# Optimization experiments

Measured on AMD Instinct MI355X. Metric: run time of the kernel, lower is better.

Reference implementation:

```python
import jax, jax.numpy as jnp
import numpy as np

B, S, U, V, L = 64, 2048, 1024, 50257, 8
RESIDUAL = (False, False, True, True, True, True, True, False)


def setup_inputs() -> dict:
    key = jax.random.key(0)
    ks = jax.random.split(key, 8)
    sc = 0.02
    return {
        "enc_output": jax.random.normal(ks[0], (B, S, U), jnp.float32),
        "dec_input": jax.random.normal(ks[1], (B, 1, U), jnp.float32),
        "query_h": jax.random.normal(ks[2], (B, U), jnp.float32),
        "attn_W1": jax.random.normal(ks[3], (U, U), jnp.float32) * sc,
        "attn_b1": jnp.zeros((U,), jnp.float32),
        "attn_W2": jax.random.normal(ks[4], (U, U), jnp.float32) * sc,
        "attn_b2": jnp.zeros((U,), jnp.float32),
        "attn_V": jax.random.normal(ks[5], (U, 1), jnp.float32) * sc,
        "attn_bV": jnp.zeros((1,), jnp.float32),
        "lstm_W": jax.random.normal(ks[6], (L, 2 * U, 4 * U), jnp.float32) * sc,
        "lstm_b": jnp.zeros((L, 4 * U), jnp.float32),
        "dense_W": jax.random.normal(ks[7], (U, V), jnp.float32) * sc,
        "dense_b": jnp.zeros((V,), jnp.float32),
    }


def reference(enc_output, dec_input, query_h, attn_W1, attn_b1, attn_W2, attn_b2,
              attn_V, attn_bV, lstm_W, lstm_b, dense_W, dense_b):
    # Bahdanau attention: score over the S (time) axis of enc_output
    feat = jnp.tanh(jnp.einsum('bsu,uv->bsv', enc_output, attn_W1) + attn_b1
                    + (query_h @ attn_W2 + attn_b2)[:, None, :])          # [B,S,U]
    score = jnp.einsum('bsu,uo->bso', feat, attn_V) + attn_bV             # [B,S,1]
    attn_w = jax.nn.softmax(score, axis=1)                                # [B,S,1]
    ctx = jnp.sum(attn_w * enc_output, axis=1)                            # [B,U]

    # 8 stacked single-step LSTMs. NOTE: original code never passes
    # initial_state, so h_prev = c_prev = 0 and the recurrent kernel
    # contributes exactly zero for a length-1 sequence.
    x = dec_input[:, 0, :]                                                # [B,U]
    hs, cs = [], []
    for i in range(L):
        inp = jnp.concatenate([x, ctx], axis=-1)                          # [B,2U]
        z = inp @ lstm_W[i] + lstm_b[i]                                   # [B,4U]
        i_g, f_g, g_g, o_g = jnp.split(z, 4, axis=-1)                     # keras order i,f,c,o
        c = jax.nn.sigmoid(i_g) * jnp.tanh(g_g)                           # f*c_prev == 0
        h = jax.nn.sigmoid(o_g) * jnp.tanh(c)
        hs.append(h)
        cs.append(c)
        x = h + inp[:, :U] if RESIDUAL[i] else h                          # residual on layers 2..6

    logits = x @ dense_W + dense_b                                        # [B,V]
    probs = jax.nn.softmax(logits, axis=-1)[:, None, :]                   # [B,1,V]
    return probs, jnp.stack(hs), jnp.stack(cs), attn_w
```

## Files before the change

kernel.cpp:

```cpp
#include <hip/hip_runtime.h>
#include <stdint.h>

#define B_  64
#define S_  2048
#define U_  1024
#define V_  50257
#define L_  8

typedef __attribute__((ext_vector_type(4))) float  f32x4;
typedef __attribute__((ext_vector_type(8))) short  bf16x8;
typedef __attribute__((ext_vector_type(4))) unsigned short us4;

__device__ inline unsigned short f2bf(float f){
  union { float f; unsigned u; } x; x.f = f;
  unsigned r = (x.u + 0x7FFFu + ((x.u >> 16) & 1u)) >> 16;
  return (unsigned short)r;
}
__device__ inline float fast_tanh(float x){
  float e = __expf(2.0f * x);
  return (e - 1.0f) * __builtin_amdgcn_rcpf(e + 1.0f);
}
__device__ inline void gload_lds16(const void* g, void* l){
  __builtin_amdgcn_global_load_lds(
      (const __attribute__((address_space(1))) unsigned int*)g,
      (__attribute__((address_space(3))) unsigned int*)l, 16, 0, 0);
}

__global__ void k1a_w1t(const float* __restrict__ W1, unsigned short* __restrict__ W1T){
  __shared__ float tile[64][65];
  int bu = blockIdx.x & 15, bv = blockIdx.x >> 4;
  int u0 = bu * 64, v0 = bv * 64;
  int t = threadIdx.x;
  int r = t >> 6, c = t & 63;
  #pragma unroll 4
  for (int it = 0; it < 16; ++it){
    int rr = it * 4 + r;
    tile[rr][c] = W1[(long)(u0 + rr) * 1024 + v0 + c];
  }
  __syncthreads();
  #pragma unroll 4
  for (int it = 0; it < 16; ++it){
    int vr = it * 4 + r;
    W1T[(long)(v0 + vr) * 1024 + u0 + c] = f2bf(tile[c][vr]);
  }
}

__global__ void k1b_qbias(const float* __restrict__ qh, const float* __restrict__ W2,
                          const float* __restrict__ b1, const float* __restrict__ b2,
                          float* __restrict__ qbias){
  int b = blockIdx.x >> 2;
  int v = (blockIdx.x & 3) * 256 + threadIdx.x;
  const float* qr = qh + b * 1024;
  float a = 0.f;
  for (int j = 0; j < 256; ++j){
    f32x4 qv = *(const f32x4*)(qr + j * 4);
    a += qv[0] * W2[(long)(j*4+0)*1024 + v] + qv[1] * W2[(long)(j*4+1)*1024 + v]
       + qv[2] * W2[(long)(j*4+2)*1024 + v] + qv[3] * W2[(long)(j*4+3)*1024 + v];
  }
  qbias[b * 1024 + v] = a + b1[v] + b2[v];
}

#define K2T 512
__global__ __launch_bounds__(K2T, 2) void k2_feat_score(
    const float* __restrict__ enc, const unsigned short* __restrict__ W1T,
    const float* __restrict__ qbias, const float* __restrict__ attnV,
    float* __restrict__ score){
  __shared__ __attribute__((aligned(16))) unsigned short Bs[1024 * 64];
  __shared__ __attribute__((aligned(16))) unsigned short As[64 * 136];
  __shared__ float qbL[1024], vwL[1024], scoreL[64];

  const int tid  = threadIdx.x;
  const int lane = tid & 63;
  const int w    = tid >> 6;
  const int blk  = blockIdx.x;
  const long row0 = (long)blk * 64;
  const int b = blk >> 5;

  for (int i = tid; i < 1024; i += K2T){ qbL[i] = qbias[b*1024 + i]; vwL[i] = attnV[i]; }
  if (tid < 64) scoreL[tid] = 0.0f;

  f32x4 acc[4][8];
  #pragma unroll
  for (int mi = 0; mi < 4; ++mi)
    #pragma unroll
    for (int ni = 0; ni < 8; ++ni) acc[mi][ni] = (f32x4){0.f,0.f,0.f,0.f};

  int goff[16];
  #pragma unroll
  for (int it = 0; it < 16; ++it){
    int d = it * 512 + tid;
    int v = d >> 3, c = d & 7;
    goff[it] = v * 1024 + (c ^ (v & 7)) * 8;
  }

  for (int p = 0; p < 8; ++p){
    __syncthreads();
    {
      const float* src = enc + row0 * 1024 + p * 128;
      #pragma unroll
      for (int it = 0; it < 4; ++it){
        int idx = it * 512 + tid;
        int r = idx >> 5, c4 = idx & 31;
        f32x4 v4 = *(const f32x4*)(src + (long)r * 1024 + c4 * 4);
        us4 sv;
        sv[0] = f2bf(v4[0]); sv[1] = f2bf(v4[1]); sv[2] = f2bf(v4[2]); sv[3] = f2bf(v4[3]);
        *(us4*)&As[r * 136 + c4 * 4] = sv;
      }
    }
    #pragma unroll
    for (int s2 = 0; s2 < 2; ++s2){
      __syncthreads();
      const int kk = p * 128 + s2 * 64;
      #pragma unroll
      for (int it = 0; it < 16; ++it){
        int dbase = it * 512 + w * 64;
        gload_lds16(W1T + goff[it] + kk, &Bs[dbase * 8]);
      }
      __syncthreads();
      #pragma unroll
      for (int k0 = 0; k0 < 2; ++k0){
        bf16x8 af[4];
        #pragma unroll
        for (int mi = 0; mi < 4; ++mi){
          int r = mi * 16 + (lane & 15);
          int kloc = s2 * 64 + k0 * 32 + (lane >> 4) * 8;
          af[mi] = *(const bf16x8*)&As[r * 136 + kloc];
        }
        #pragma unroll
        for (int ni = 0; ni < 8; ++ni){
          int v = w * 128 + ni * 16 + (lane & 15);
          int c = k0 * 4 + (lane >> 4);
          bf16x8 bf = *(const bf16x8*)&Bs[v * 64 + (c ^ (v & 7)) * 8];
          #pragma unroll
          for (int mi = 0; mi < 4; ++mi)
            acc[mi][ni] = __builtin_amdgcn_mfma_f32_16x16x32_bf16(af[mi], bf, acc[mi][ni], 0, 0, 0);
        }
      }
    }
  }
  float qv[8], vv[8];
  #pragma unroll
  for (int ni = 0; ni < 8; ++ni){
    int col = w * 128 + ni * 16 + (lane & 15);
    qv[ni] = qbL[col]; vv[ni] = vwL[col];
  }
  #pragma unroll
  for (int mi = 0; mi < 4; ++mi){
    #pragma unroll
    for (int r = 0; r < 4; ++r){
      float t = 0.f;
      #pragma unroll
      for (int ni = 0; ni < 8; ++ni)
        t += fast_tanh(acc[mi][ni][r] + qv[ni]) * vv[ni];
      #pragma unroll
      for (int off = 1; off < 16; off <<= 1) t += __shfl_xor(t, off, 16);
      if ((lane & 15) == 0)
        atomicAdd(&scoreL[mi * 16 + (lane >> 4) * 4 + r], t);
    }
  }
  __syncthreads();
  if (tid < 64) score[row0 + tid] = scoreL[tid];
}

__global__ void k3_softmax_s(const float* __restrict__ score, float* __restrict__ attnw){
  __shared__ float red[256];
  int b = blockIdx.x, t = threadIdx.x;
  const float* sc = score + b * 2048;
  float m = -1e30f;
  for (int i = t; i < 2048; i += 256) m = fmaxf(m, sc[i]);
  red[t] = m; __syncthreads();
  for (int s = 128; s > 0; s >>= 1){ if (t < s) red[t] = fmaxf(red[t], red[t+s]); __syncthreads(); }
  float M = red[0]; __syncthreads();
  float p = 0.f;
  for (int i = t; i < 2048; i += 256) p += __expf(sc[i] - M);
  red[t] = p; __syncthreads();
  for (int s = 128; s > 0; s >>= 1){ if (t < s) red[t] += red[t+s]; __syncthreads(); }
  float inv = 1.0f / red[0];
  for (int i = t; i < 2048; i += 256) attnw[b * 2048 + i] = __expf(sc[i] - M) * inv;
}

__global__ void k4_ctx(const float* __restrict__ enc, const float* __restrict__ attnw,
                       float* __restrict__ ctx){
  __shared__ float wL[2048];
  __shared__ f32x4 red[8][32];
  int b = blockIdx.x >> 3, uc = blockIdx.x & 7;
  int t = threadIdx.x;
  for (int i = t; i < 2048; i += 256) wL[i] = attnw[b * 2048 + i];
  __syncthreads();
  int g = t >> 5, l32 = t & 31;
  const float* base = enc + (long)b * 2048 * 1024 + uc * 128 + l32 * 4;
  f32x4 a = (f32x4){0.f,0.f,0.f,0.f};
  for (int s = g; s < 2048; s += 8){
    f32x4 e = *(const f32x4*)(base + (long)s * 1024);
    a += e * wL[s];
  }
  red[g][l32] = a; __syncthreads();
  if (g == 0){
    f32x4 r = red[0][l32];
    #pragma unroll
    for (int i = 1; i < 8; ++i) r += red[i][l32];
    *(f32x4*)(ctx + b * 1024 + uc * 128 + l32 * 4) = r;
  }
}

__global__ void k5a_gemm(const float* __restrict__ x, const float* __restrict__ ctx,
                         const float* __restrict__ W, float* __restrict__ zpart){
  __shared__ float inpL[64 * 256];
  int blk = blockIdx.x;
  int nc = blk % 48, ks = blk / 48;
  int t = threadIdx.x;
  int gc = (nc < 16) ? nc * 64 : (nc < 32 ? 2048 + (nc - 16) * 64 : 3072 + (nc - 32) * 64);
  const float* ib = (ks < 4) ? x : ctx;
  int koff = (ks & 3) * 256;
  #pragma unroll 4
  for (int it = 0; it < 16; ++it){
    int idx = it * 256 + t;
    int r = idx >> 6, c4 = idx & 63;
    *(f32x4*)&inpL[r * 256 + c4 * 4] = *(const f32x4*)(ib + (long)r * 1024 + koff + c4 * 4);
  }
  __syncthreads();
  int b4 = (t & 15) * 4, n4 = (t >> 4) * 4;
  f32x4 a0 = (f32x4){0,0,0,0}, a1 = a0, a2 = a0, a3 = a0;
  const float* Wb = W + (long)(ks * 256) * 4096 + gc + n4;
  #pragma unroll 2
  for (int j = 0; j < 64; ++j){
    f32x4 w0 = *(const f32x4*)(Wb + (long)(j*4+0) * 4096);
    f32x4 w1 = *(const f32x4*)(Wb + (long)(j*4+1) * 4096);
    f32x4 w2 = *(const f32x4*)(Wb + (long)(j*4+2) * 4096);
    f32x4 w3 = *(const f32x4*)(Wb + (long)(j*4+3) * 4096);
    f32x4 x0 = *(const f32x4*)&inpL[(b4+0) * 256 + j * 4];
    f32x4 x1 = *(const f32x4*)&inpL[(b4+1) * 256 + j * 4];
    f32x4 x2 = *(const f32x4*)&inpL[(b4+2) * 256 + j * 4];
    f32x4 x3 = *(const f32x4*)&inpL[(b4+3) * 256 + j * 4];
    a0 += w0*x0[0]; a0 += w1*x0[1]; a0 += w2*x0[2]; a0 += w3*x0[3];
    a1 += w0*x1[0]; a1 += w1*x1[1]; a1 += w2*x1[2]; a1 += w3*x1[3];
    a2 += w0*x2[0]; a2 += w1*x2[1]; a2 += w2*x2[2]; a2 += w3*x2[3];
    a3 += w0*x3[0]; a3 += w1*x3[1]; a3 += w2*x3[2]; a3 += w3*x3[3];
  }
  float* zp = zpart + (long)ks * 64 * 3072 + nc * 64 + n4;
  *(f32x4*)(zp + (long)(b4+0) * 3072) = a0;
  *(f32x4*)(zp + (long)(b4+1) * 3072) = a1;
  *(f32x4*)(zp + (long)(b4+2) * 3072) = a2;
  *(f32x4*)(zp + (long)(b4+3) * 3072) = a3;
}

__global__ void k5b_gates(const float* __restrict__ zpart, const float* __restrict__ lb,
                          const float* __restrict__ xin, float* __restrict__ xout,
                          float* __restrict__ hs, float* __restrict__ cs, int resid){
  int b = blockIdx.x, t = threadIdx.x;
  int n4 = t * 4;
  f32x4 zi = (f32x4){0,0,0,0}, zg = zi, zo = zi;
  #pragma unroll
  for (int ks = 0; ks < 8; ++ks){
    const float* zp = zpart + (long)ks * 64 * 3072 + b * 3072;
    zi += *(const f32x4*)(zp + n4);
    zg += *(const f32x4*)(zp + 1024 + n4);
    zo += *(const f32x4*)(zp + 2048 + n4);
  }
  zi += *(const f32x4*)(lb + n4);
  zg += *(const f32x4*)(lb + 2048 + n4);
  zo += *(const f32x4*)(lb + 3072 + n4);
  f32x4 c, h;
  #pragma unroll
  for (int j = 0; j < 4; ++j){
    float cv = (1.f / (1.f + __expf(-zi[j]))) * tanhf(zg[j]);
    float hv = (1.f / (1.f + __expf(-zo[j]))) * tanhf(cv);
    c[j] = cv; h[j] = hv;
  }
  f32x4 xn = h;
  if (resid) xn += *(const f32x4*)(xin + b * 1024 + n4);
  *(f32x4*)(hs + b * 1024 + n4) = h;
  *(f32x4*)(cs + b * 1024 + n4) = c;
  *(f32x4*)(xout + b * 1024 + n4) = xn;
}

__global__ void k6_dense(const float* __restrict__ x, const float* __restrict__ dW,
                         const float* __restrict__ db, float* __restrict__ logits){
  int nc = blockIdx.x, t = threadIdx.x;
  int b4 = (t & 15) * 4, nl = (t >> 4) * 4;
  int col = nc * 64 + nl;
  int c0 = min(col + 0, V_ - 1), c1 = min(col + 1, V_ - 1);
  int c2 = min(col + 2, V_ - 1), c3 = min(col + 3, V_ - 1);
  f32x4 a[4];
  #pragma unroll
  for (int bi = 0; bi < 4; ++bi) a[bi] = (f32x4){0,0,0,0};
  for (int j = 0; j < 256; ++j){
    f32x4 xv0 = *(const f32x4*)(x + (long)(b4+0) * 1024 + j * 4);
    f32x4 xv1 = *(const f32x4*)(x + (long)(b4+1) * 1024 + j * 4);
    f32x4 xv2 = *(const f32x4*)(x + (long)(b4+2) * 1024 + j * 4);
    f32x4 xv3 = *(const f32x4*)(x + (long)(b4+3) * 1024 + j * 4);
    #pragma unroll
    for (int ki = 0; ki < 4; ++ki){
      const float* wr = dW + (long)(j * 4 + ki) * V_;
      f32x4 wv = { wr[c0], wr[c1], wr[c2], wr[c3] };
      a[0] += wv * xv0[ki]; a[1] += wv * xv1[ki];
      a[2] += wv * xv2[ki]; a[3] += wv * xv3[ki];
    }
  }
  f32x4 bias = { db[c0], db[c1], db[c2], db[c3] };
  #pragma unroll
  for (int bi = 0; bi < 4; ++bi){
    f32x4 r = a[bi] + bias;
    #pragma unroll
    for (int j = 0; j < 4; ++j)
      if (col + j < V_) logits[(long)(b4 + bi) * V_ + col + j] = r[j];
  }
}

__global__ void k7_softmax_v(const float* __restrict__ logits, float* __restrict__ probs){
  __shared__ float red[1024];
  int b = blockIdx.x, t = threadIdx.x;
  const float* lg = logits + (long)b * V_;
  float* pr = probs + (long)b * V_;
  float m = -1e30f;
  for (int i = t; i < V_; i += 1024) m = fmaxf(m, lg[i]);
  red[t] = m; __syncthreads();
  for (int s = 512; s > 0; s >>= 1){ if (t < s) red[t] = fmaxf(red[t], red[t+s]); __syncthreads(); }
  float M = red[0]; __syncthreads();
  float p = 0.f;
  for (int i = t; i < V_; i += 1024){ float e = __expf(lg[i] - M); pr[i] = e; p += e; }
  red[t] = p; __syncthreads();
  for (int s = 512; s > 0; s >>= 1){ if (t < s) red[t] += red[t+s]; __syncthreads(); }
  float inv = 1.0f / red[0];
  for (int i = t; i < V_; i += 1024) pr[i] *= inv;
}

extern "C" void kernel_launch(void* const* d_in, const int* in_sizes, int n_in,
                              void* d_out, int out_size, void* d_ws, size_t ws_size,
                              hipStream_t stream){
  const float* enc = (const float*)d_in[0];
  const float* dec = (const float*)d_in[1];
  const float* qh  = (const float*)d_in[2];
  const float* W1  = (const float*)d_in[3];
  const float* b1  = (const float*)d_in[4];
  const float* W2  = (const float*)d_in[5];
  const float* b2  = (const float*)d_in[6];
  const float* aV  = (const float*)d_in[7];
  const float* lW  = (const float*)d_in[9];
  const float* lb  = (const float*)d_in[10];
  const float* dW  = (const float*)d_in[11];
  const float* db  = (const float*)d_in[12];

  float* out   = (float*)d_out;
  float* probs = out;
  float* hs    = out + 3216448;
  float* cs    = out + 3740736;
  float* attnw = out + 4265024;

  char* ws = (char*)d_ws;
  unsigned short* W1T = (unsigned short*)(ws + 0);
  float* score  = (float*)(ws + 2097152);
  float* qbias  = (float*)(ws + 2621440);
  float* ctx    = (float*)(ws + 2883584);
  float* xbuf   = (float*)(ws + 3145728);
  float* zpart  = (float*)(ws + 3407872);
  float* logits = (float*)(ws + 9699328);

  hipLaunchKernelGGL(k1a_w1t,      dim3(256),  dim3(256),  0, stream, W1, W1T);
  hipLaunchKernelGGL(k1b_qbias,    dim3(256),  dim3(256),  0, stream, qh, W2, b1, b2, qbias);
  hipLaunchKernelGGL(k2_feat_score,dim3(2048), dim3(K2T),  0, stream, enc, W1T, qbias, aV, score);
  hipLaunchKernelGGL(k3_softmax_s, dim3(64),   dim3(256),  0, stream, score, attnw);
  hipLaunchKernelGGL(k4_ctx,       dim3(512),  dim3(256),  0, stream, enc, attnw, ctx);

  static const int RES[8] = {0,0,1,1,1,1,1,0};
  const float* xin = dec;
  for (int i = 0; i < 8; ++i){
    hipLaunchKernelGGL(k5a_gemm,  dim3(384), dim3(256), 0, stream,
                       xin, ctx, lW + (long)i * 2048 * 4096, zpart);
    hipLaunchKernelGGL(k5b_gates, dim3(64),  dim3(256), 0, stream,
                       zpart, lb + i * 4096, xin, xbuf,
                       hs + i * 65536, cs + i * 65536, RES[i]);
    xin = xbuf;
  }
  hipLaunchKernelGGL(k6_dense,     dim3(786), dim3(256),  0, stream, xbuf, dW, db, logits);
  hipLaunchKernelGGL(k7_softmax_v, dim3(64),  dim3(1024), 0, stream, logits, probs);
}
```

Baseline: 2.898 ms.

## Double-buffer attention GEMM, repack W1 tiles, split ctx reduction, retile dense

The attention feature GEMM now double-buffers A and B tiles in LDS with K-step 32. The next tile's W1 load (direct-to-LDS) and the enc row load are issued while the MFMAs on the current tile run, and there is one barrier per step. W1 is pre-packed into contiguous swizzled 32-wide K tiles so each step reads a linear block. The context reduction is split over S chunks with a second reduce kernel, and the dense layer is retiled so each thread computes 16 batch rows for one column with coalesced weight reads. zpart and logits now share workspace, which relies on the two never being live at the same time.

Result: faster. 2.516 ms (-13.2%).

```diff
diff --git a/kernel.cpp b/kernel.cpp
--- a/kernel.cpp
+++ b/kernel.cpp
@@ -10,6 +10,7 @@
 typedef __attribute__((ext_vector_type(4))) float  f32x4;
 typedef __attribute__((ext_vector_type(8))) short  bf16x8;
 typedef __attribute__((ext_vector_type(4))) unsigned short us4;
+typedef __attribute__((ext_vector_type(8))) unsigned short us8;
 
 __device__ inline unsigned short f2bf(float f){
   union { float f; unsigned u; } x; x.f = f;
@@ -26,22 +27,28 @@
       (__attribute__((address_space(3))) unsigned int*)l, 16, 0, 0);
 }
 
-__global__ void k1a_w1t(const float* __restrict__ W1, unsigned short* __restrict__ W1T){
-  __shared__ float tile[64][65];
-  int bu = blockIdx.x & 15, bv = blockIdx.x >> 4;
-  int u0 = bu * 64, v0 = bv * 64;
+__global__ void k1a_w1b(const float* __restrict__ W1, unsigned short* __restrict__ W1B){
+  __shared__ float tile[32][257];
+  int tt = blockIdx.x >> 2;
+  int v0 = (blockIdx.x & 3) * 256;
   int t = threadIdx.x;
-  int r = t >> 6, c = t & 63;
   #pragma unroll 4
-  for (int it = 0; it < 16; ++it){
-    int rr = it * 4 + r;
-    tile[rr][c] = W1[(long)(u0 + rr) * 1024 + v0 + c];
-  }
-  __syncthreads();
-  #pragma unroll 4
-  for (int it = 0; it < 16; ++it){
-    int vr = it * 4 + r;
-    W1T[(long)(v0 + vr) * 1024 + u0 + c] = f2bf(tile[c][vr]);
+  for (int i = 0; i < 32; ++i){
+    int idx = i * 256 + t;
+    int r = idx >> 8, c = idx & 255;
+    tile[r][c] = W1[(long)(tt * 32 + r) * 1024 + v0 + c];
+  }
+  __syncthreads();
+  #pragma unroll
+  for (int i = 0; i < 4; ++i){
+    int gid = i * 256 + t;
+    int vl = gid >> 2, cp = gid & 3;
+    int v = v0 + vl;
+    int chunk = cp ^ ((v >> 1) & 3);
+    us8 o;
+    #pragma unroll
+    for (int e = 0; e < 8; ++e) o[e] = f2bf(tile[chunk * 8 + e][vl]);
+    *(us8*)&W1B[((long)(tt * 1024 + v) * 4 + cp) * 8] = o;
   }
 }
 
@@ -62,21 +69,19 @@
 
 #define K2T 512
 __global__ __launch_bounds__(K2T, 2) void k2_feat_score(
-    const float* __restrict__ enc, const unsigned short* __restrict__ W1T,
+    const float* __restrict__ enc, const unsigned short* __restrict__ W1B,
     const float* __restrict__ qbias, const float* __restrict__ attnV,
     float* __restrict__ score){
-  __shared__ __attribute__((aligned(16))) unsigned short Bs[1024 * 64];
-  __shared__ __attribute__((aligned(16))) unsigned short As[64 * 136];
-  __shared__ float qbL[1024], vwL[1024], scoreL[64];
+  __shared__ __attribute__((aligned(16))) unsigned short Bs[2][1024 * 32];
+  __shared__ __attribute__((aligned(16))) unsigned short As[2][64 * 40];
+  __shared__ float scoreL[64];
 
   const int tid  = threadIdx.x;
   const int lane = tid & 63;
   const int w    = tid >> 6;
-  const int blk  = blockIdx.x;
-  const long row0 = (long)blk * 64;
-  const int b = blk >> 5;
-
-  for (int i = tid; i < 1024; i += K2T){ qbL[i] = qbias[b*1024 + i]; vwL[i] = attnV[i]; }
+  const long row0 = (long)blockIdx.x * 64;
+  const int b = blockIdx.x >> 5;
+
   if (tid < 64) scoreL[tid] = 0.0f;
 
   f32x4 acc[4][8];
@@ -85,64 +90,59 @@
     #pragma unroll
     for (int ni = 0; ni < 8; ++ni) acc[mi][ni] = (f32x4){0.f,0.f,0.f,0.f};
 
-  int goff[16];
-  #pragma unroll
-  for (int it = 0; it < 16; ++it){
-    int d = it * 512 + tid;
-    int v = d >> 3, c = d & 7;
-    goff[it] = v * 1024 + (c ^ (v & 7)) * 8;
-  }
-
-  for (int p = 0; p < 8; ++p){
+  const int ar = tid >> 3, ac4 = tid & 7;
+  const float* aptr = enc + (row0 + ar) * 1024 + ac4 * 4;
+  const int aoff = ar * 40 + ac4 * 4;
+
+  #pragma unroll
+  for (int i = 0; i < 8; ++i)
+    gload_lds16(W1B + (i * 512 + tid) * 8, &Bs[0][(i * 512 + w * 64) * 8]);
+  {
+    f32x4 av = *(const f32x4*)(aptr);
+    us4 sv; sv[0]=f2bf(av[0]); sv[1]=f2bf(av[1]); sv[2]=f2bf(av[2]); sv[3]=f2bf(av[3]);
+    *(us4*)&As[0][aoff] = sv;
+  }
+  __syncthreads();
+
+  int cur = 0;
+  for (int t = 0; t < 32; ++t){
+    const int nxt = cur ^ 1;
+    f32x4 av = (f32x4){0.f,0.f,0.f,0.f};
+    if (t < 31){
+      const long bbase = (long)(t + 1) * 32768;
+      #pragma unroll
+      for (int i = 0; i < 8; ++i)
+        gload_lds16(W1B + bbase + (i * 512 + tid) * 8, &Bs[nxt][(i * 512 + w * 64) * 8]);
+      av = *(const f32x4*)(aptr + (t + 1) * 32);
+    }
+    bf16x8 af[4];
+    #pragma unroll
+    for (int mi = 0; mi < 4; ++mi){
+      int r = mi * 16 + (lane & 15);
+      af[mi] = *(const bf16x8*)&As[cur][r * 40 + (lane >> 4) * 8];
+    }
+    #pragma unroll
+    for (int ni = 0; ni < 8; ++ni){
+      int v = w * 128 + ni * 16 + (lane & 15);
+      int cp = (lane >> 4) ^ ((v >> 1) & 3);
+      bf16x8 bf = *(const bf16x8*)&Bs[cur][v * 32 + cp * 8];
+      #pragma unroll
+      for (int mi = 0; mi < 4; ++mi)
+        acc[mi][ni] = __builtin_amdgcn_mfma_f32_16x16x32_bf16(af[mi], bf, acc[mi][ni], 0, 0, 0);
+    }
+    if (t < 31){
+      us4 sv; sv[0]=f2bf(av[0]); sv[1]=f2bf(av[1]); sv[2]=f2bf(av[2]); sv[3]=f2bf(av[3]);
+      *(us4*)&As[nxt][aoff] = sv;
+    }
     __syncthreads();
-    {
-      const float* src = enc + row0 * 1024 + p * 128;
-      #pragma unroll
-      for (int it = 0; it < 4; ++it){
-        int idx = it * 512 + tid;
-        int r = idx >> 5, c4 = idx & 31;
-        f32x4 v4 = *(const f32x4*)(src + (long)r * 1024 + c4 * 4);
-        us4 sv;
-        sv[0] = f2bf(v4[0]); sv[1] = f2bf(v4[1]); sv[2] = f2bf(v4[2]); sv[3] = f2bf(v4[3]);
-        *(us4*)&As[r * 136 + c4 * 4] = sv;
-      }
-    }
-    #pragma unroll
-    for (int s2 = 0; s2 < 2; ++s2){
-      __syncthreads();
-      const int kk = p * 128 + s2 * 64;
-      #pragma unroll
-      for (int it = 0; it < 16; ++it){
-        int dbase = it * 512 + w * 64;
-        gload_lds16(W1T + goff[it] + kk, &Bs[dbase * 8]);
-      }
-      __syncthreads();
-      #pragma unroll
-      for (int k0 = 0; k0 < 2; ++k0){
-        bf16x8 af[4];
-        #pragma unroll
-        for (int mi = 0; mi < 4; ++mi){
-          int r = mi * 16 + (lane & 15);
-          int kloc = s2 * 64 + k0 * 32 + (lane >> 4) * 8;
-          af[mi] = *(const bf16x8*)&As[r * 136 + kloc];
-        }
-        #pragma unroll
-        for (int ni = 0; ni < 8; ++ni){
-          int v = w * 128 + ni * 16 + (lane & 15);
-          int c = k0 * 4 + (lane >> 4);
-          bf16x8 bf = *(const bf16x8*)&Bs[v * 64 + (c ^ (v & 7)) * 8];
-          #pragma unroll
-          for (int mi = 0; mi < 4; ++mi)
-            acc[mi][ni] = __builtin_amdgcn_mfma_f32_16x16x32_bf16(af[mi], bf, acc[mi][ni], 0, 0, 0);
-        }
-      }
-    }
-  }
+    cur = nxt;
+  }
+
   float qv[8], vv[8];
   #pragma unroll
   for (int ni = 0; ni < 8; ++ni){
     int col = w * 128 + ni * 16 + (lane & 15);
-    qv[ni] = qbL[col]; vv[ni] = vwL[col];
+    qv[ni] = qbias[b * 1024 + col]; vv[ni] = attnV[col];
   }
   #pragma unroll
   for (int mi = 0; mi < 4; ++mi){
@@ -179,28 +179,28 @@
   for (int i = t; i < 2048; i += 256) attnw[b * 2048 + i] = __expf(sc[i] - M) * inv;
 }
 
-__global__ void k4_ctx(const float* __restrict__ enc, const float* __restrict__ attnw,
-                       float* __restrict__ ctx){
-  __shared__ float wL[2048];
-  __shared__ f32x4 red[8][32];
-  int b = blockIdx.x >> 3, uc = blockIdx.x & 7;
+__global__ void k4a_ctxp(const float* __restrict__ enc, const float* __restrict__ attnw,
+                         float* __restrict__ ctxp){
+  __shared__ float wL[256];
+  int b = blockIdx.x >> 3, sc = blockIdx.x & 7;
   int t = threadIdx.x;
-  for (int i = t; i < 2048; i += 256) wL[i] = attnw[b * 2048 + i];
-  __syncthreads();
-  int g = t >> 5, l32 = t & 31;
-  const float* base = enc + (long)b * 2048 * 1024 + uc * 128 + l32 * 4;
+  wL[t] = attnw[b * 2048 + sc * 256 + t];
+  __syncthreads();
+  const float* base = enc + ((long)b * 2048 + sc * 256) * 1024 + t * 4;
   f32x4 a = (f32x4){0.f,0.f,0.f,0.f};
-  for (int s = g; s < 2048; s += 8){
-    f32x4 e = *(const f32x4*)(base + (long)s * 1024);
-    a += e * wL[s];
-  }
-  red[g][l32] = a; __syncthreads();
-  if (g == 0){
-    f32x4 r = red[0][l32];
-    #pragma unroll
-    for (int i = 1; i < 8; ++i) r += red[i][l32];
-    *(f32x4*)(ctx + b * 1024 + uc * 128 + l32 * 4) = r;
-  }
+  #pragma unroll 4
+  for (int s = 0; s < 256; ++s)
+    a += (*(const f32x4*)(base + (long)s * 1024)) * wL[s];
+  *(f32x4*)(ctxp + ((long)(sc * 64 + b)) * 1024 + t * 4) = a;
+}
+
+__global__ void k4b_ctx(const float* __restrict__ ctxp, float* __restrict__ ctx){
+  int b = blockIdx.x, t = threadIdx.x;
+  f32x4 a = (f32x4){0.f,0.f,0.f,0.f};
+  #pragma unroll
+  for (int sc = 0; sc < 8; ++sc)
+    a += *(const f32x4*)(ctxp + ((long)(sc * 64 + b)) * 1024 + t * 4);
+  *(f32x4*)(ctx + b * 1024 + t * 4) = a;
 }
 
 __global__ void k5a_gemm(const float* __restrict__ x, const float* __restrict__ ctx,
@@ -274,36 +274,34 @@
   *(f32x4*)(xout + b * 1024 + n4) = xn;
 }
 
-__global__ void k6_dense(const float* __restrict__ x, const float* __restrict__ dW,
+__global__ __launch_bounds__(256) void k6_dense(const float* __restrict__ x, const float* __restrict__ dW,
                          const float* __restrict__ db, float* __restrict__ logits){
-  int nc = blockIdx.x, t = threadIdx.x;
-  int b4 = (t & 15) * 4, nl = (t >> 4) * 4;
-  int col = nc * 64 + nl;
-  int c0 = min(col + 0, V_ - 1), c1 = min(col + 1, V_ - 1);
-  int c2 = min(col + 2, V_ - 1), c3 = min(col + 3, V_ - 1);
-  f32x4 a[4];
-  #pragma unroll
-  for (int bi = 0; bi < 4; ++bi) a[bi] = (f32x4){0,0,0,0};
-  for (int j = 0; j < 256; ++j){
-    f32x4 xv0 = *(const f32x4*)(x + (long)(b4+0) * 1024 + j * 4);
-    f32x4 xv1 = *(const f32x4*)(x + (long)(b4+1) * 1024 + j * 4);
-    f32x4 xv2 = *(const f32x4*)(x + (long)(b4+2) * 1024 + j * 4);
-    f32x4 xv3 = *(const f32x4*)(x + (long)(b4+3) * 1024 + j * 4);
-    #pragma unroll
-    for (int ki = 0; ki < 4; ++ki){
-      const float* wr = dW + (long)(j * 4 + ki) * V_;
-      f32x4 wv = { wr[c0], wr[c1], wr[c2], wr[c3] };
-      a[0] += wv * xv0[ki]; a[1] += wv * xv1[ki];
-      a[2] += wv * xv2[ki]; a[3] += wv * xv3[ki];
-    }
-  }
-  f32x4 bias = { db[c0], db[c1], db[c2], db[c3] };
-  #pragma unroll
-  for (int bi = 0; bi < 4; ++bi){
-    f32x4 r = a[bi] + bias;
-    #pragma unroll
-    for (int j = 0; j < 4; ++j)
-      if (col + j < V_) logits[(long)(b4 + bi) * V_ + col + j] = r[j];
+  int t = threadIdx.x;
+  int cl = t & 63, bg = t >> 6;
+  int col = blockIdx.x * 64 + cl;
+  int colc = min(col, V_ - 1);
+  float acc[16];
+  #pragma unroll
+  for (int bi = 0; bi < 16; ++bi) acc[bi] = 0.f;
+  const float* xb = x + (long)bg * 16 * 1024;
+  for (int k4 = 0; k4 < 256; ++k4){
+    f32x4 xv[16];
+    #pragma unroll
+    for (int bi = 0; bi < 16; ++bi)
+      xv[bi] = *(const f32x4*)(xb + (long)bi * 1024 + k4 * 4);
+    #pragma unroll
+    for (int j = 0; j < 4; ++j){
+      float wv = dW[((long)k4 * 4 + j) * V_ + colc];
+      #pragma unroll
+      for (int bi = 0; bi < 16; ++bi)
+        acc[bi] += xv[bi][j] * wv;
+    }
+  }
+  if (col < V_){
+    float bias = db[colc];
+    #pragma unroll
+    for (int bi = 0; bi < 16; ++bi)
+      logits[(long)(bg * 16 + bi) * V_ + col] = acc[bi] + bias;
   }
 }
 
@@ -348,19 +346,21 @@
   float* attnw = out + 4265024;
 
   char* ws = (char*)d_ws;
-  unsigned short* W1T = (unsigned short*)(ws + 0);
+  unsigned short* W1B = (unsigned short*)(ws + 0);
   float* score  = (float*)(ws + 2097152);
   float* qbias  = (float*)(ws + 2621440);
   float* ctx    = (float*)(ws + 2883584);
   float* xbuf   = (float*)(ws + 3145728);
-  float* zpart  = (float*)(ws + 3407872);
-  float* logits = (float*)(ws + 9699328);
-
-  hipLaunchKernelGGL(k1a_w1t,      dim3(256),  dim3(256),  0, stream, W1, W1T);
+  float* ctxp   = (float*)(ws + 3407872);
+  float* zpart  = (float*)(ws + 5505024);
+  float* logits = (float*)(ws + 5505024);
+
+  hipLaunchKernelGGL(k1a_w1b,      dim3(128),  dim3(256),  0, stream, W1, W1B);
   hipLaunchKernelGGL(k1b_qbias,    dim3(256),  dim3(256),  0, stream, qh, W2, b1, b2, qbias);
-  hipLaunchKernelGGL(k2_feat_score,dim3(2048), dim3(K2T),  0, stream, enc, W1T, qbias, aV, score);
+  hipLaunchKernelGGL(k2_feat_score,dim3(2048), dim3(K2T),  0, stream, enc, W1B, qbias, aV, score);
   hipLaunchKernelGGL(k3_softmax_s, dim3(64),   dim3(256),  0, stream, score, attnw);
-  hipLaunchKernelGGL(k4_ctx,       dim3(512),  dim3(256),  0, stream, enc, attnw, ctx);
+  hipLaunchKernelGGL(k4a_ctxp,     dim3(512),  dim3(256),  0, stream, enc, attnw, ctxp);
+  hipLaunchKernelGGL(k4b_ctx,      dim3(64),   dim3(256),  0, stream, ctxp, ctx);
 
   static const int RES[8] = {0,0,1,1,1,1,1,0};
   const float* xin = dec;
```
